# Optimization experiments

Hardware: AMD Instinct MI355X
Metric: run time of the kernel (lower is better)

The kernel has to match this reference:

```python
import jax, jax.numpy as jnp
import numpy as np

N_NODES = 150000
N_EDGES = 3000000
EMBED_DIM = 64
N_LAYERS = 3


def setup_inputs() -> dict:
    key = jax.random.key(0)
    k1, k2, k3, k4 = jax.random.split(key, 4)
    emb = jax.random.normal(k1, (N_NODES, EMBED_DIM), dtype=jnp.float32)
    sqrt_degree = jax.random.uniform(k2, (N_NODES, 1), dtype=jnp.float32)
    src = jax.random.randint(k3, (N_EDGES,), 0, N_NODES, dtype=jnp.int32)
    dst = jax.random.randint(k4, (N_EDGES,), 0, N_NODES, dtype=jnp.int32)
    return {"emb": emb, "sqrt_degree": sqrt_degree, "src": src, "dst": dst}


def _aggregate_unweighted(x, sqrt_degree, src, dst):
    # node = x * sqrt_degree ; message = node[src] ; N_h = sum per dst ; N_h *= sqrt_degree
    scaled = x * sqrt_degree                      # [N, D]
    msgs = scaled[src]                            # [E, D] gather
    agg = jax.ops.segment_sum(msgs, dst, num_segments=N_NODES)  # [N, D] scatter-add
    return agg * sqrt_degree


def reference(emb, sqrt_degree, src, dst):
    # propagate_embedding: ego embedding + n_layers of symmetric-normalized SpMM,
    # mean-combined across layers (layers_weight is None -> plain mean).
    ego = emb
    all_embed = [ego]
    for _ in range(N_LAYERS):
        ego = _aggregate_unweighted(ego, sqrt_degree, src, dst)
        all_embed.append(ego)
    return jnp.mean(jnp.stack(all_embed, axis=-1), axis=-1)  # [N, D]
```

## Files before the change

kernel.cpp:

```cpp
#include <hip/hip_runtime.h>

#define N_NODES   150000
#define N_EDGES   3000000
#define EMBED_DIM 64
#define N_UNITS   (N_EDGES / 4)
#define NREG      2344
#define CHUNK_U   2048
#define CHUNK_E   (CHUNK_U * 4)
#define NCB       ((N_UNITS + CHUNK_U - 1) / CHUNK_U)
#define REC_MAX   2560
#define CAP       2560
#define UPT       4

typedef unsigned int uint;

__device__ inline uint pack2_bf16(float a, float b) {
    uint ua = __float_as_uint(a);
    uint ub = __float_as_uint(b);
    ua += 0x7fffu + ((ua >> 16) & 1u);
    ub += 0x7fffu + ((ub >> 16) & 1u);
    return (ua >> 16) | (ub & 0xffff0000u);
}
__device__ inline float bflo(uint u) { return __uint_as_float(u << 16); }
__device__ inline float bfhi(uint u) { return __uint_as_float(u & 0xffff0000u); }
#define FMA2(u, A0, A1)                                        \
    {   (A0) += w * bflo(u);  (A1) += w * bfhi(u); }

__global__ __launch_bounds__(512) void k_count_place(const int4* __restrict__ dst4,
                                                     const int4* __restrict__ src4,
                                                     uint* __restrict__ bh,
                                                     uint* __restrict__ rowtot,
                                                     uint* __restrict__ bkt) {
    __shared__ uint cnt[NREG];
    __shared__ uint part[512];
    int t = threadIdx.x;
    for (int b = t; b < NREG; b += 512) cnt[b] = 0;
    __syncthreads();
    int base = blockIdx.x * CHUNK_U;

    uint rec[UPT * 4];
    uint reg[UPT * 4];
    #pragma unroll
    for (int it = 0; it < UPT; ++it) {
        int u = base + t + it * 512;
        if (u < N_UNITS) {
            int4 d = dst4[u];
            int4 s = src4[u];
            reg[it * 4 + 0] = (uint)d.x >> 6;  rec[it * 4 + 0] = ((uint)s.x << 6) | ((uint)d.x & 63u);
            reg[it * 4 + 1] = (uint)d.y >> 6;  rec[it * 4 + 1] = ((uint)s.y << 6) | ((uint)d.y & 63u);
            reg[it * 4 + 2] = (uint)d.z >> 6;  rec[it * 4 + 2] = ((uint)s.z << 6) | ((uint)d.z & 63u);
            reg[it * 4 + 3] = (uint)d.w >> 6;  rec[it * 4 + 3] = ((uint)s.w << 6) | ((uint)d.w & 63u);
            atomicAdd(&cnt[reg[it * 4 + 0]], 1u);
            atomicAdd(&cnt[reg[it * 4 + 1]], 1u);
            atomicAdd(&cnt[reg[it * 4 + 2]], 1u);
            atomicAdd(&cnt[reg[it * 4 + 3]], 1u);
        } else {
            reg[it * 4 + 0] = 0xFFFFFFFFu; reg[it * 4 + 1] = 0xFFFFFFFFu;
            reg[it * 4 + 2] = 0xFFFFFFFFu; reg[it * 4 + 3] = 0xFFFFFFFFu;
        }
    }
    __syncthreads();
    const int CPT = (NREG + 511) / 512;
    int b0 = t * CPT, b1 = b0 + CPT; if (b1 > NREG) b1 = NREG; if (b0 > NREG) b0 = NREG;
    uint own = 0;
    for (int b = b0; b < b1; ++b) own += cnt[b];
    part[t] = own;
    __syncthreads();
    for (int off = 1; off < 512; off <<= 1) {
        uint v = (t >= off) ? part[t - off] : 0;
        __syncthreads();
        part[t] += v;
        __syncthreads();
    }
    uint run = part[t] - own;
    for (int b = b0; b < b1; ++b) { uint c = cnt[b]; cnt[b] = run; run += c; }
    __syncthreads();
    for (int b = t; b < NREG; b += 512) bh[blockIdx.x * NREG + b] = cnt[b];
    if (t == 511) rowtot[blockIdx.x] = part[511];
    __syncthreads();
    uint kbase = (uint)blockIdx.x * CHUNK_E;
    #pragma unroll
    for (int q = 0; q < UPT * 4; ++q) {
        if (reg[q] != 0xFFFFFFFFu) {
            uint pos = atomicAdd(&cnt[reg[q]], 1u);
            bkt[kbase + pos] = rec[q];
        }
    }
}

__global__ __launch_bounds__(256) void k_finalize(const uint* __restrict__ bkt,
                                                  const uint* __restrict__ bh,
                                                  const uint* __restrict__ rowtot,
                                                  const float4* __restrict__ emb4,
                                                  const float* __restrict__ sd,
                                                  int2* __restrict__ rowse,
                                                  uint* __restrict__ srcn,
                                                  uint2* __restrict__ y0) {
    __shared__ uint recs[REC_MAX];
    __shared__ uint part[256];
    __shared__ uint cnt64[64];
    __shared__ uint off64[65];
    int r = blockIdx.x;
    int t = threadIdx.x;
    int rbase = r * CAP;
    int nbase = r * 64;
    int nloc = N_NODES - nbase; if (nloc > 64) nloc = 64;

    int k0 = 2 * t, k1 = 2 * t + 1;
    uint s0 = 0, c0 = 0, s1 = 0, c1 = 0;
    if (k0 < NCB) {
        s0 = bh[k0 * NREG + r];
        uint e0 = (r + 1 < NREG) ? bh[k0 * NREG + r + 1] : rowtot[k0];
        c0 = e0 - s0;
    }
    if (k1 < NCB) {
        s1 = bh[k1 * NREG + r];
        uint e1 = (r + 1 < NREG) ? bh[k1 * NREG + r + 1] : rowtot[k1];
        c1 = e1 - s1;
    }
    uint own = c0 + c1;
    part[t] = own;
    __syncthreads();
    for (int off = 1; off < 256; off <<= 1) {
        uint v = (t >= off) ? part[t - off] : 0;
        __syncthreads();
        part[t] += v;
        __syncthreads();
    }
    int rcnt = (int)part[255];
    uint w0 = part[t] - own;
    uint w1 = w0 + c0;
    for (uint i = 0; i < c0; ++i) recs[w0 + i] = bkt[(uint)k0 * CHUNK_E + s0 + i];
    for (uint i = 0; i < c1; ++i) recs[w1 + i] = bkt[(uint)k1 * CHUNK_E + s1 + i];
    if (t < 64) cnt64[t] = 0;
    __syncthreads();

    for (int e = t; e < rcnt; e += 256) atomicAdd(&cnt64[recs[e] & 63u], 1u);
    __syncthreads();
    if (t == 0) {
        uint run = 0;
        for (int i = 0; i < 64; ++i) { off64[i] = run; run += cnt64[i]; }
        off64[64] = run;
    }
    __syncthreads();
    if (t < nloc)
        rowse[nbase + t] = make_int2(rbase + (int)off64[t], rbase + (int)off64[t + 1]);
    if (t < 64) cnt64[t] = 0;
    __syncthreads();

    for (int e = t; e < rcnt; e += 256) {
        uint rec = recs[e];
        uint loc = rec & 63u;
        uint pos = (uint)rbase + off64[loc] + atomicAdd(&cnt64[loc], 1u);
        srcn[pos] = rec >> 6;
    }

    for (int i = t; i < nloc * 16; i += 256) {
        int gi = nbase * 16 + i;
        float s = sd[nbase + (i >> 4)];
        float4 v = emb4[gi];
        y0[gi] = make_uint2(pack2_bf16(s * v.x, s * v.y), pack2_bf16(s * v.z, s * v.w));
    }
}

__global__ __launch_bounds__(256) void k_layer(const uint4* __restrict__ yb,
                                               const int2* __restrict__ rowse,
                                               const uint* __restrict__ srcn,
                                               const float* __restrict__ sd,
                                               uint4* __restrict__ yout) {
    int wv = (blockIdx.x * blockDim.x + threadIdx.x) >> 6;
    wv = __builtin_amdgcn_readfirstlane(wv);
    int nA = wv * 2;
    if (nA >= N_NODES) return;
    int nB = nA + 1;
    int lane = threadIdx.x & 63;
    int ep = lane >> 3;
    int j  = lane & 7;
    uint joff = (uint)j << 4;

    int2 rA = rowse[nA];
    int2 rB = rowse[nB];
    int startA = rA.x, endA = rA.y;
    int startB = rB.x, endB = rB.y;
    int eAm1 = max(endA - 1, 0);
    int eBm1 = max(endB - 1, 0);

    float a0 = 0.f, a1 = 0.f, a2 = 0.f, a3 = 0.f;
    float a4 = 0.f, a5 = 0.f, a6 = 0.f, a7 = 0.f;
    float b0 = 0.f, b1 = 0.f, b2 = 0.f, b3 = 0.f;
    float b4 = 0.f, b5 = 0.f, b6 = 0.f, b7 = 0.f;
    #pragma unroll 2
    for (int bA = startA, bB = startB; bA < endA || bB < endB; bA += 8, bB += 8) {
        int eeA = bA + ep;
        int eeB = bB + ep;
        int ecA = min(eeA, eAm1);
        int ecB = min(eeB, eBm1);
        uint sA = min(srcn[ecA], (uint)(N_NODES - 1));
        uint sB = min(srcn[ecB], (uint)(N_NODES - 1));
        float wA = (eeA < endA) ? 1.0f : 0.0f;
        float wB = (eeB < endB) ? 1.0f : 0.0f;
        uint4 vA = *(const uint4*)((const char*)yb + ((sA << 7) + joff));
        uint4 vB = *(const uint4*)((const char*)yb + ((sB << 7) + joff));
        { float w = wA;
          FMA2(vA.x, a0, a1); FMA2(vA.y, a2, a3); FMA2(vA.z, a4, a5); FMA2(vA.w, a6, a7); }
        { float w = wB;
          FMA2(vB.x, b0, b1); FMA2(vB.y, b2, b3); FMA2(vB.z, b4, b5); FMA2(vB.w, b6, b7); }
    }
    #pragma unroll
    for (int m = 8; m <= 32; m <<= 1) {
        a0 += __shfl_xor(a0, m, 64); a1 += __shfl_xor(a1, m, 64);
        a2 += __shfl_xor(a2, m, 64); a3 += __shfl_xor(a3, m, 64);
        a4 += __shfl_xor(a4, m, 64); a5 += __shfl_xor(a5, m, 64);
        a6 += __shfl_xor(a6, m, 64); a7 += __shfl_xor(a7, m, 64);
        b0 += __shfl_xor(b0, m, 64); b1 += __shfl_xor(b1, m, 64);
        b2 += __shfl_xor(b2, m, 64); b3 += __shfl_xor(b3, m, 64);
        b4 += __shfl_xor(b4, m, 64); b5 += __shfl_xor(b5, m, 64);
        b6 += __shfl_xor(b6, m, 64); b7 += __shfl_xor(b7, m, 64);
    }
    if (ep == 0) {
        float sdv = sd[nA];
        float s2 = sdv * sdv;
        uint4 r;
        r.x = pack2_bf16(s2 * a0, s2 * a1);
        r.y = pack2_bf16(s2 * a2, s2 * a3);
        r.z = pack2_bf16(s2 * a4, s2 * a5);
        r.w = pack2_bf16(s2 * a6, s2 * a7);
        yout[(size_t)nA * 8 + j] = r;
    } else if (ep == 1) {
        float sdv = sd[nB];
        float s2 = sdv * sdv;
        uint4 r;
        r.x = pack2_bf16(s2 * b0, s2 * b1);
        r.y = pack2_bf16(s2 * b2, s2 * b3);
        r.z = pack2_bf16(s2 * b4, s2 * b5);
        r.w = pack2_bf16(s2 * b6, s2 * b7);
        yout[(size_t)nB * 8 + j] = r;
    }
}

__global__ __launch_bounds__(256) void k_layer_final(const uint4* __restrict__ y2b,
                                                     const uint4* __restrict__ y1b,
                                                     const float4* __restrict__ emb,
                                                     const int2* __restrict__ rowse,
                                                     const uint* __restrict__ srcn,
                                                     const float* __restrict__ sd,
                                                     float4* __restrict__ out) {
    int wv = (blockIdx.x * blockDim.x + threadIdx.x) >> 6;
    wv = __builtin_amdgcn_readfirstlane(wv);
    int nA = wv * 2;
    if (nA >= N_NODES) return;
    int nB = nA + 1;
    int lane = threadIdx.x & 63;
    int ep = lane >> 3;
    int j  = lane & 7;
    uint joff = (uint)j << 4;

    int2 rA = rowse[nA];
    int2 rB = rowse[nB];
    int startA = rA.x, endA = rA.y;
    int startB = rB.x, endB = rB.y;
    int eAm1 = max(endA - 1, 0);
    int eBm1 = max(endB - 1, 0);

    float a0 = 0.f, a1 = 0.f, a2 = 0.f, a3 = 0.f;
    float a4 = 0.f, a5 = 0.f, a6 = 0.f, a7 = 0.f;
    float b0 = 0.f, b1 = 0.f, b2 = 0.f, b3 = 0.f;
    float b4 = 0.f, b5 = 0.f, b6 = 0.f, b7 = 0.f;
    #pragma unroll 2
    for (int bA = startA, bB = startB; bA < endA || bB < endB; bA += 8, bB += 8) {
        int eeA = bA + ep;
        int eeB = bB + ep;
        int ecA = min(eeA, eAm1);
        int ecB = min(eeB, eBm1);
        uint sA = min(srcn[ecA], (uint)(N_NODES - 1));
        uint sB = min(srcn[ecB], (uint)(N_NODES - 1));
        float wA = (eeA < endA) ? 1.0f : 0.0f;
        float wB = (eeB < endB) ? 1.0f : 0.0f;
        uint4 vA = *(const uint4*)((const char*)y2b + ((sA << 7) + joff));
        uint4 vB = *(const uint4*)((const char*)y2b + ((sB << 7) + joff));
        { float w = wA;
          FMA2(vA.x, a0, a1); FMA2(vA.y, a2, a3); FMA2(vA.z, a4, a5); FMA2(vA.w, a6, a7); }
        { float w = wB;
          FMA2(vB.x, b0, b1); FMA2(vB.y, b2, b3); FMA2(vB.z, b4, b5); FMA2(vB.w, b6, b7); }
    }
    #pragma unroll
    for (int m = 8; m <= 32; m <<= 1) {
        a0 += __shfl_xor(a0, m, 64); a1 += __shfl_xor(a1, m, 64);
        a2 += __shfl_xor(a2, m, 64); a3 += __shfl_xor(a3, m, 64);
        a4 += __shfl_xor(a4, m, 64); a5 += __shfl_xor(a5, m, 64);
        a6 += __shfl_xor(a6, m, 64); a7 += __shfl_xor(a7, m, 64);
        b0 += __shfl_xor(b0, m, 64); b1 += __shfl_xor(b1, m, 64);
        b2 += __shfl_xor(b2, m, 64); b3 += __shfl_xor(b3, m, 64);
        b4 += __shfl_xor(b4, m, 64); b5 += __shfl_xor(b5, m, 64);
        b6 += __shfl_xor(b6, m, 64); b7 += __shfl_xor(b7, m, 64);
    }
    int nd; float t0, t1, t2, t3, t4, t5, t6, t7;
    bool emit = false;
    if (ep == 0) {
        nd = nA; emit = true;
        t0 = a0; t1 = a1; t2 = a2; t3 = a3; t4 = a4; t5 = a5; t6 = a6; t7 = a7;
    } else if (ep == 1) {
        nd = nB; emit = true;
        t0 = b0; t1 = b1; t2 = b2; t3 = b3; t4 = b4; t5 = b5; t6 = b6; t7 = b7;
    }
    if (emit) {
        float sdv  = sd[nd];
        float rinv = (sdv > 0.0f) ? 1.0f / sdv : 0.0f;
        size_t ridx = (size_t)nd * 8 + j;
        uint4 u1 = y1b[ridx];
        uint4 u2 = y2b[ridx];
        float q0 = (bflo(u1.x) + bflo(u2.x)) * rinv + sdv * t0;
        float q1 = (bfhi(u1.x) + bfhi(u2.x)) * rinv + sdv * t1;
        float q2 = (bflo(u1.y) + bflo(u2.y)) * rinv + sdv * t2;
        float q3 = (bfhi(u1.y) + bfhi(u2.y)) * rinv + sdv * t3;
        float q4 = (bflo(u1.z) + bflo(u2.z)) * rinv + sdv * t4;
        float q5 = (bfhi(u1.z) + bfhi(u2.z)) * rinv + sdv * t5;
        float q6 = (bflo(u1.w) + bflo(u2.w)) * rinv + sdv * t6;
        float q7 = (bfhi(u1.w) + bfhi(u2.w)) * rinv + sdv * t7;
        size_t eidx = (size_t)nd * 16 + (size_t)j * 2;
        float4 e0 = emb[eidx];
        float4 e1 = emb[eidx + 1];
        float4 o0 = make_float4(0.25f * (e0.x + q0), 0.25f * (e0.y + q1),
                                0.25f * (e0.z + q2), 0.25f * (e0.w + q3));
        float4 o1 = make_float4(0.25f * (e1.x + q4), 0.25f * (e1.y + q5),
                                0.25f * (e1.z + q6), 0.25f * (e1.w + q7));
        out[eidx]     = o0;
        out[eidx + 1] = o1;
    }
}

extern "C" void kernel_launch(void* const* d_in, const int* in_sizes, int n_in,
                              void* d_out, int out_size, void* d_ws, size_t ws_size,
                              hipStream_t stream) {
    const float* emb = (const float*)d_in[0];
    const float* sd  = (const float*)d_in[1];
    const int*   src = (const int*)d_in[2];
    const int*   dst = (const int*)d_in[3];
    float*       out = (float*)d_out;

    char* ws = (char*)d_ws;
    auto align256 = [](size_t x) { return (x + 255) & ~(size_t)255; };
    size_t off = 0;
    int2* rowse  = (int2*)(ws + off); off += align256((size_t)N_NODES * 8);
    uint* bh     = (uint*)(ws + off); off += align256((size_t)NCB * NREG * 4);
    uint* rowtot = (uint*)(ws + off); off += align256((size_t)NCB * 4);
    uint* bkt    = (uint*)(ws + off); off += align256((size_t)NCB * CHUNK_E * 4);
    uint* srcn   = (uint*)(ws + off); off += align256((size_t)NREG * CAP * 4);
    const size_t rowBytes = (size_t)N_NODES * EMBED_DIM * 2;
    uint* buf0 = (uint*)(ws + off);   off += align256(rowBytes);
    uint* buf1 = (uint*)(ws + off);   off += align256(rowBytes);
    uint* buf2 = (uint*)(ws + off);

    k_count_place<<<NCB, 512, 0, stream>>>((const int4*)dst, (const int4*)src,
                                           bh, rowtot, bkt);
    k_finalize<<<NREG, 256, 0, stream>>>(bkt, bh, rowtot, (const float4*)emb, sd,
                                         rowse, srcn, (uint2*)buf0);

    const int nwaves = (N_NODES + 1) / 2;
    const int lblk = (nwaves + 3) / 4;
    k_layer<<<lblk, 256, 0, stream>>>((const uint4*)buf0, rowse, srcn, sd, (uint4*)buf1);
    k_layer<<<lblk, 256, 0, stream>>>((const uint4*)buf1, rowse, srcn, sd, (uint4*)buf2);
    k_layer_final<<<lblk, 256, 0, stream>>>((const uint4*)buf2, (const uint4*)buf1,
                                            (const float4*)emb, rowse, srcn, sd,
                                            (float4*)out);
}
```

Measured before the change: 240.5 us.

## Sort per-node edge lists by source slice and widen count/place blocks to 1024

In k_finalize, each destination node's edges are now bucketed into 10 coarse source-id slices (rec>>20, about 16K nodes each), so neighbor lists come out partially sorted by source. The intent is better cache locality for the gathers in the three layer kernels. Separately, k_count_place goes from 512 to 1024 threads per block with fewer units per thread, which raises parallelism but makes the scan longer. The serial prefix over 640 counters done by a single thread adds latency to the finalize step.

After: 252.8 us. 1.05x slower.

```diff
diff --git a/kernel.cpp b/kernel.cpp
--- a/kernel.cpp
+++ b/kernel.cpp
@@ -10,7 +10,9 @@
 #define NCB       ((N_UNITS + CHUNK_U - 1) / CHUNK_U)
 #define REC_MAX   2560
 #define CAP       2560
-#define UPT       4
+#define CPB       1024
+#define UPT2      (CHUNK_U / CPB)
+#define NSLICE    10
 
 typedef unsigned int uint;
 
@@ -26,23 +28,23 @@
 #define FMA2(u, A0, A1)                                        \
     {   (A0) += w * bflo(u);  (A1) += w * bfhi(u); }
 
-__global__ __launch_bounds__(512) void k_count_place(const int4* __restrict__ dst4,
-                                                     const int4* __restrict__ src4,
-                                                     uint* __restrict__ bh,
-                                                     uint* __restrict__ rowtot,
-                                                     uint* __restrict__ bkt) {
+__global__ __launch_bounds__(1024) void k_count_place(const int4* __restrict__ dst4,
+                                                      const int4* __restrict__ src4,
+                                                      uint* __restrict__ bh,
+                                                      uint* __restrict__ rowtot,
+                                                      uint* __restrict__ bkt) {
     __shared__ uint cnt[NREG];
-    __shared__ uint part[512];
+    __shared__ uint part[CPB];
     int t = threadIdx.x;
-    for (int b = t; b < NREG; b += 512) cnt[b] = 0;
+    for (int b = t; b < NREG; b += CPB) cnt[b] = 0;
     __syncthreads();
     int base = blockIdx.x * CHUNK_U;
 
-    uint rec[UPT * 4];
-    uint reg[UPT * 4];
+    uint rec[UPT2 * 4];
+    uint reg[UPT2 * 4];
     #pragma unroll
-    for (int it = 0; it < UPT; ++it) {
-        int u = base + t + it * 512;
+    for (int it = 0; it < UPT2; ++it) {
+        int u = base + t + it * CPB;
         if (u < N_UNITS) {
             int4 d = dst4[u];
             int4 s = src4[u];
@@ -60,13 +62,13 @@
         }
     }
     __syncthreads();
-    const int CPT = (NREG + 511) / 512;
+    const int CPT = (NREG + CPB - 1) / CPB;
     int b0 = t * CPT, b1 = b0 + CPT; if (b1 > NREG) b1 = NREG; if (b0 > NREG) b0 = NREG;
     uint own = 0;
     for (int b = b0; b < b1; ++b) own += cnt[b];
     part[t] = own;
     __syncthreads();
-    for (int off = 1; off < 512; off <<= 1) {
+    for (int off = 1; off < CPB; off <<= 1) {
         uint v = (t >= off) ? part[t - off] : 0;
         __syncthreads();
         part[t] += v;
@@ -75,12 +77,12 @@
     uint run = part[t] - own;
     for (int b = b0; b < b1; ++b) { uint c = cnt[b]; cnt[b] = run; run += c; }
     __syncthreads();
-    for (int b = t; b < NREG; b += 512) bh[blockIdx.x * NREG + b] = cnt[b];
-    if (t == 511) rowtot[blockIdx.x] = part[511];
+    for (int b = t; b < NREG; b += CPB) bh[blockIdx.x * NREG + b] = cnt[b];
+    if (t == CPB - 1) rowtot[blockIdx.x] = part[CPB - 1];
     __syncthreads();
     uint kbase = (uint)blockIdx.x * CHUNK_E;
     #pragma unroll
-    for (int q = 0; q < UPT * 4; ++q) {
+    for (int q = 0; q < UPT2 * 4; ++q) {
         if (reg[q] != 0xFFFFFFFFu) {
             uint pos = atomicAdd(&cnt[reg[q]], 1u);
             bkt[kbase + pos] = rec[q];
@@ -98,7 +100,7 @@
                                                   uint2* __restrict__ y0) {
     __shared__ uint recs[REC_MAX];
     __shared__ uint part[256];
-    __shared__ uint cnt64[64];
+    __shared__ uint cnt640[64 * NSLICE];
     __shared__ uint off64[65];
     int r = blockIdx.x;
     int t = threadIdx.x;
@@ -132,26 +134,35 @@
     uint w1 = w0 + c0;
     for (uint i = 0; i < c0; ++i) recs[w0 + i] = bkt[(uint)k0 * CHUNK_E + s0 + i];
     for (uint i = 0; i < c1; ++i) recs[w1 + i] = bkt[(uint)k1 * CHUNK_E + s1 + i];
-    if (t < 64) cnt64[t] = 0;
-    __syncthreads();
-
-    for (int e = t; e < rcnt; e += 256) atomicAdd(&cnt64[recs[e] & 63u], 1u);
+    for (int i = t; i < 64 * NSLICE; i += 256) cnt640[i] = 0;
+    __syncthreads();
+
+    for (int e = t; e < rcnt; e += 256) {
+        uint rec = recs[e];
+        atomicAdd(&cnt640[(rec & 63u) * NSLICE + (rec >> 20)], 1u);
+    }
     __syncthreads();
     if (t == 0) {
         uint run = 0;
-        for (int i = 0; i < 64; ++i) { off64[i] = run; run += cnt64[i]; }
+        for (int loc = 0; loc < 64; ++loc) {
+            off64[loc] = run;
+            #pragma unroll
+            for (int sl = 0; sl < NSLICE; ++sl) {
+                uint c = cnt640[loc * NSLICE + sl];
+                cnt640[loc * NSLICE + sl] = run;
+                run += c;
+            }
+        }
         off64[64] = run;
     }
     __syncthreads();
     if (t < nloc)
         rowse[nbase + t] = make_int2(rbase + (int)off64[t], rbase + (int)off64[t + 1]);
-    if (t < 64) cnt64[t] = 0;
     __syncthreads();
 
     for (int e = t; e < rcnt; e += 256) {
         uint rec = recs[e];
-        uint loc = rec & 63u;
-        uint pos = (uint)rbase + off64[loc] + atomicAdd(&cnt64[loc], 1u);
+        uint pos = (uint)rbase + atomicAdd(&cnt640[(rec & 63u) * NSLICE + (rec >> 20)], 1u);
         srcn[pos] = rec >> 6;
     }
 
@@ -351,7 +362,7 @@
     uint* buf1 = (uint*)(ws + off);   off += align256(rowBytes);
     uint* buf2 = (uint*)(ws + off);
 
-    k_count_place<<<NCB, 512, 0, stream>>>((const int4*)dst, (const int4*)src,
+    k_count_place<<<NCB, CPB, 0, stream>>>((const int4*)dst, (const int4*)src,
                                            bh, rowtot, bkt);
     k_finalize<<<NREG, 256, 0, stream>>>(bkt, bh, rowtot, (const float4*)emb, sd,
                                          rowse, srcn, (uint2*)buf0);
```
